# Performance work log

Hardware: AMD Instinct MI355X
Metric: run time of the kernel (lower is better)

## Reference

```python
import jax, jax.numpy as jnp
import numpy as np

B, T, U = 4, 512, 100
A_FEAT, TXT_FEAT, HID, NCLS = 512, 320, 640, 512


def setup_inputs() -> dict:
    key = jax.random.key(0)
    ks = jax.random.split(key, 8)
    s = lambda fan_in: 1.0 / np.sqrt(fan_in)
    return {
        "audio_frame": jax.random.normal(ks[0], (B, T, A_FEAT), jnp.float32),
        "text_frame": jax.random.normal(ks[1], (B, U, TXT_FEAT), jnp.float32),
        "W_a": jax.random.uniform(ks[2], (A_FEAT, HID), jnp.float32, -s(A_FEAT), s(A_FEAT)),
        "b_a": jax.random.uniform(ks[3], (HID,), jnp.float32, -s(A_FEAT), s(A_FEAT)),
        "W_t": jax.random.uniform(ks[4], (TXT_FEAT, HID), jnp.float32, -s(TXT_FEAT), s(TXT_FEAT)),
        "b_t": jax.random.uniform(ks[5], (HID,), jnp.float32, -s(TXT_FEAT), s(TXT_FEAT)),
        "W_j": jax.random.uniform(ks[6], (HID, NCLS), jnp.float32, -s(HID), s(HID)),
        "b_j": jax.random.uniform(ks[7], (NCLS,), jnp.float32, -s(HID), s(HID)),
    }


def reference(audio_frame, text_frame, W_a, b_a, W_t, b_t, W_j, b_j):
    # [B,T,H] and [B,U,H] projections
    a = jnp.einsum("bta,ah->bth", audio_frame, W_a) + b_a
    t = jnp.einsum("bux,xh->buh", text_frame, W_t) + b_t
    # broadcast add -> [B,T,U,H], tanh, final linear -> [B,T,U,V]
    joint = jnp.tanh(a[:, :, None, :] + t[:, None, :, :])
    return jnp.einsum("btuh,hv->btuv", joint, W_j) + b_j
```

## Files before the change

kernel.cpp:

```cpp
#include <hip/hip_runtime.h>
#include <hip/hip_bf16.h>
#include <stdint.h>

#define BB   4
#define TT   512
#define UU   100
#define AF   512
#define TXF  320
#define HID  640
#define NCLS 512
#define TU   (TT * UU)
#define M3   (BB * TU)

typedef unsigned short ushort_t;
typedef __attribute__((ext_vector_type(8))) short frag_ab;
typedef __attribute__((ext_vector_type(4))) float frag_cd;
typedef __attribute__((ext_vector_type(8))) unsigned short ushort8;

__device__ __forceinline__ float bf2f(unsigned short h) {
    return __uint_as_float(((unsigned)h) << 16);
}
__device__ __forceinline__ unsigned short f2bf(float f) {
    unsigned u = __float_as_uint(f);
    u += 0x7FFFu + ((u >> 16) & 1u);
    return (unsigned short)(u >> 16);
}
__device__ __forceinline__ float tanh_fast(float x) {
    float e = __expf(2.0f * x);
    return 1.0f - 2.0f * __builtin_amdgcn_rcpf(e + 1.0f);
}

__global__ void tcast_kernel(const float* __restrict__ src, ushort_t* __restrict__ dst,
                             int K, int N) {
    int i = blockIdx.x * 256 + threadIdx.x;
    if (i >= K * N) return;
    int k = i / N;
    int n = i - k * N;
    dst[n * K + k] = f2bf(src[i]);
}

__global__ __launch_bounds__(256) void proj_kernel(
    const float* __restrict__ X, const ushort_t* __restrict__ Wt,
    const float* __restrict__ bias, ushort_t* __restrict__ P,
    int M, int K)
{
    __shared__ ushort_t As[128][72];
    __shared__ ushort_t Bs[128][72];
    int tid = threadIdx.x;
    int m0 = blockIdx.x * 128, n0 = blockIdx.y * 128;
    int wave = tid >> 6, lane = tid & 63;
    int wr = (wave >> 1) * 64, wc = (wave & 1) * 64;
    int lm = lane & 15, lq = lane >> 4;
    frag_cd acc[4][4];
    #pragma unroll
    for (int i = 0; i < 4; ++i)
        #pragma unroll
        for (int j = 0; j < 4; ++j) { frag_cd z = {0.f, 0.f, 0.f, 0.f}; acc[i][j] = z; }
    int rs = tid >> 3, k8 = tid & 7;

    for (int k0 = 0; k0 < K; k0 += 64) {
        #pragma unroll
        for (int it = 0; it < 4; ++it) {
            int r = rs + it * 32;
            int m = m0 + r;
            float4 v0 = make_float4(0.f, 0.f, 0.f, 0.f), v1 = v0;
            if (m < M) {
                const float* xp = X + (size_t)m * K + (k0 + k8 * 8);
                v0 = *(const float4*)xp;
                v1 = *(const float4*)(xp + 4);
            }
            ushort8 o;
            o[0] = f2bf(v0.x); o[1] = f2bf(v0.y); o[2] = f2bf(v0.z); o[3] = f2bf(v0.w);
            o[4] = f2bf(v1.x); o[5] = f2bf(v1.y); o[6] = f2bf(v1.z); o[7] = f2bf(v1.w);
            *(ushort8*)&As[r][k8 * 8] = o;
            uint4 w = *(const uint4*)(Wt + (size_t)(n0 + r) * K + (k0 + k8 * 8));
            *(uint4*)&Bs[r][k8 * 8] = w;
        }
        __syncthreads();
        #pragma unroll
        for (int kk = 0; kk < 64; kk += 32) {
            frag_ab af[4], bfr[4];
            #pragma unroll
            for (int i = 0; i < 4; ++i) af[i]  = *(const frag_ab*)&As[wr + i * 16 + lm][kk + lq * 8];
            #pragma unroll
            for (int j = 0; j < 4; ++j) bfr[j] = *(const frag_ab*)&Bs[wc + j * 16 + lm][kk + lq * 8];
            #pragma unroll
            for (int i = 0; i < 4; ++i)
                #pragma unroll
                for (int j = 0; j < 4; ++j)
                    acc[i][j] = __builtin_amdgcn_mfma_f32_16x16x32_bf16(af[i], bfr[j], acc[i][j], 0, 0, 0);
        }
        __syncthreads();
    }
    #pragma unroll
    for (int j = 0; j < 4; ++j) {
        int n = n0 + wc + j * 16 + lm;
        float bv = bias[n];
        #pragma unroll
        for (int i = 0; i < 4; ++i) {
            int mb = m0 + wr + i * 16 + lq * 4;
            #pragma unroll
            for (int r = 0; r < 4; ++r) {
                int m = mb + r;
                if (m < M) P[(size_t)m * HID + n] = f2bf(acc[i][j][r] + bv);
            }
        }
    }
}

__global__ __launch_bounds__(256, 2) void joint_kernel(
    const ushort_t* __restrict__ Pa, const ushort_t* __restrict__ Pt,
    const ushort_t* __restrict__ Wtj, const float* __restrict__ bj,
    float* __restrict__ out)
{
    __shared__ ushort_t As[128][72];
    __shared__ ushort_t Bs[256][72];
    __shared__ int aOff[128];
    __shared__ int tOff[128];
    int tid = threadIdx.x;
    int m0 = blockIdx.x * 128;
    int n0 = blockIdx.y * 256;
    if (tid < 128) {
        int m  = m0 + tid;
        int b  = m / TU;
        int rb = m - b * TU;
        int ti = rb / UU;
        int ui = rb - ti * UU;
        aOff[tid] = (b * TT + ti) * HID;
        tOff[tid] = (b * UU + ui) * HID;
    }
    int wave = tid >> 6, lane = tid & 63;
    int wr = (wave >> 1) * 64;
    int wc = (wave & 1) * 128;
    int lm = lane & 15, lq = lane >> 4;
    frag_cd acc[4][8];
    #pragma unroll
    for (int i = 0; i < 4; ++i)
        #pragma unroll
        for (int j = 0; j < 8; ++j) { frag_cd z = {0.f, 0.f, 0.f, 0.f}; acc[i][j] = z; }
    int rs = tid >> 3, k8 = tid & 7;
    __syncthreads();

    for (int k0 = 0; k0 < HID; k0 += 64) {
        #pragma unroll
        for (int it = 0; it < 4; ++it) {
            int r = rs + it * 32;
            const ushort_t* ap = Pa + aOff[r] + k0 + k8 * 8;
            const ushort_t* tp = Pt + tOff[r] + k0 + k8 * 8;
            uint4 av = *(const uint4*)ap;
            uint4 tv = *(const uint4*)tp;
            const unsigned* au = (const unsigned*)&av;
            const unsigned* tu = (const unsigned*)&tv;
            ushort8 o;
            #pragma unroll
            for (int j = 0; j < 4; ++j) {
                unsigned ua = au[j], ut = tu[j];
                float s0 = __uint_as_float(ua << 16) + __uint_as_float(ut << 16);
                float s1 = __uint_as_float(ua & 0xFFFF0000u) + __uint_as_float(ut & 0xFFFF0000u);
                o[2 * j]     = f2bf(tanh_fast(s0));
                o[2 * j + 1] = f2bf(tanh_fast(s1));
            }
            *(ushort8*)&As[r][k8 * 8] = o;
        }
        #pragma unroll
        for (int it = 0; it < 8; ++it) {
            int r = rs + it * 32;
            *(uint4*)&Bs[r][k8 * 8] = *(const uint4*)(Wtj + (size_t)(n0 + r) * HID + k0 + k8 * 8);
        }
        __syncthreads();
        #pragma unroll
        for (int kk = 0; kk < 64; kk += 32) {
            frag_ab af[4], bfr[8];
            #pragma unroll
            for (int i = 0; i < 4; ++i) af[i]  = *(const frag_ab*)&As[wr + i * 16 + lm][kk + lq * 8];
            #pragma unroll
            for (int j = 0; j < 8; ++j) bfr[j] = *(const frag_ab*)&Bs[wc + j * 16 + lm][kk + lq * 8];
            #pragma unroll
            for (int i = 0; i < 4; ++i)
                #pragma unroll
                for (int j = 0; j < 8; ++j)
                    acc[i][j] = __builtin_amdgcn_mfma_f32_16x16x32_bf16(af[i], bfr[j], acc[i][j], 0, 0, 0);
        }
        __syncthreads();
    }
    #pragma unroll
    for (int j = 0; j < 8; ++j) {
        int n = n0 + wc + j * 16 + lm;
        float bv = bj[n];
        #pragma unroll
        for (int i = 0; i < 4; ++i) {
            size_t mb = (size_t)(m0 + wr + i * 16 + lq * 4);
            #pragma unroll
            for (int r = 0; r < 4; ++r) {
                out[(mb + r) * (size_t)NCLS + n] = acc[i][j][r] + bv;
            }
        }
    }
}

extern "C" void kernel_launch(void* const* d_in, const int* in_sizes, int n_in,
                              void* d_out, int out_size, void* d_ws, size_t ws_size,
                              hipStream_t stream)
{
    const float* audio = (const float*)d_in[0];
    const float* text  = (const float*)d_in[1];
    const float* Wa    = (const float*)d_in[2];
    const float* ba    = (const float*)d_in[3];
    const float* Wt    = (const float*)d_in[4];
    const float* bt    = (const float*)d_in[5];
    const float* Wj    = (const float*)d_in[6];
    const float* bjv   = (const float*)d_in[7];
    float* out = (float*)d_out;

    char* ws = (char*)d_ws;
    ushort_t* Pa  = (ushort_t*)(ws);
    ushort_t* Pt  = (ushort_t*)(ws + 2621440);
    ushort_t* Wta = (ushort_t*)(ws + 3133440);
    ushort_t* Wtt = (ushort_t*)(ws + 3788800);
    ushort_t* Wtj = (ushort_t*)(ws + 4198400);

    tcast_kernel<<<dim3((AF * HID + 255) / 256), 256, 0, stream>>>(Wa, Wta, AF, HID);
    tcast_kernel<<<dim3((TXF * HID + 255) / 256), 256, 0, stream>>>(Wt, Wtt, TXF, HID);
    tcast_kernel<<<dim3((HID * NCLS + 255) / 256), 256, 0, stream>>>(Wj, Wtj, HID, NCLS);

    proj_kernel<<<dim3(16, 5), 256, 0, stream>>>(audio, Wta, ba, Pa, BB * TT, AF);
    proj_kernel<<<dim3(4, 5), 256, 0, stream>>>(text, Wtt, bt, Pt, BB * UU, TXF);

    joint_kernel<<<dim3(M3 / 128, NCLS / 256), 256, 0, stream>>>(Pa, Pt, Wtj, bjv, out);
}
```

Measured before the change: 639.4 us.

## Cover all classes per joint block and prefetch next K tile into registers

The joint kernel now uses 512-thread blocks that cover all 512 output classes at once. The tanh(a+t) activation tile is computed once per row block instead of twice, which halves the transcendental work and the Pa/Pt gathers. Global loads for the next K slice are issued into registers before the MFMA loop runs, so load latency overlaps compute. The tanh now uses exp2 with a prescaled constant. In exchange the LDS footprint is larger and register pressure is higher under launch_bounds(512,2), so occupancy may drop.

After: 802.0 us. 25.4% more time.

```diff
diff --git a/kernel.cpp b/kernel.cpp
--- a/kernel.cpp
+++ b/kernel.cpp
@@ -26,7 +26,7 @@
     return (unsigned short)(u >> 16);
 }
 __device__ __forceinline__ float tanh_fast(float x) {
-    float e = __expf(2.0f * x);
+    float e = __builtin_amdgcn_exp2f(x * 2.8853900817779268f);
     return 1.0f - 2.0f * __builtin_amdgcn_rcpf(e + 1.0f);
 }
 
@@ -108,18 +108,17 @@
     }
 }
 
-__global__ __launch_bounds__(256, 2) void joint_kernel(
+__global__ __launch_bounds__(512, 2) void joint_kernel(
     const ushort_t* __restrict__ Pa, const ushort_t* __restrict__ Pt,
     const ushort_t* __restrict__ Wtj, const float* __restrict__ bj,
     float* __restrict__ out)
 {
     __shared__ ushort_t As[128][72];
-    __shared__ ushort_t Bs[256][72];
+    __shared__ ushort_t Bs[512][72];
     __shared__ int aOff[128];
     __shared__ int tOff[128];
     int tid = threadIdx.x;
     int m0 = blockIdx.x * 128;
-    int n0 = blockIdx.y * 256;
     if (tid < 128) {
         int m  = m0 + tid;
         int b  = m / TU;
@@ -130,8 +129,8 @@
         tOff[tid] = (b * UU + ui) * HID;
     }
     int wave = tid >> 6, lane = tid & 63;
-    int wr = (wave >> 1) * 64;
-    int wc = (wave & 1) * 128;
+    int wr = (wave >> 2) * 64;
+    int wc = (wave & 3) * 128;
     int lm = lane & 15, lq = lane >> 4;
     frag_cd acc[4][8];
     #pragma unroll
@@ -141,16 +140,26 @@
     int rs = tid >> 3, k8 = tid & 7;
     __syncthreads();
 
+    const int aO0 = aOff[rs], aO1 = aOff[rs + 64];
+    const int tO0 = tOff[rs], tO1 = tOff[rs + 64];
+    const int kcol = k8 * 8;
+
+    uint4 bv[8];
+    uint4 av[2], tv[2];
+
+    #pragma unroll
+    for (int it = 0; it < 8; ++it)
+        bv[it] = *(const uint4*)(Wtj + (size_t)(rs + it * 64) * HID + kcol);
+    av[0] = *(const uint4*)(Pa + aO0 + kcol);
+    av[1] = *(const uint4*)(Pa + aO1 + kcol);
+    tv[0] = *(const uint4*)(Pt + tO0 + kcol);
+    tv[1] = *(const uint4*)(Pt + tO1 + kcol);
+
     for (int k0 = 0; k0 < HID; k0 += 64) {
         #pragma unroll
-        for (int it = 0; it < 4; ++it) {
-            int r = rs + it * 32;
-            const ushort_t* ap = Pa + aOff[r] + k0 + k8 * 8;
-            const ushort_t* tp = Pt + tOff[r] + k0 + k8 * 8;
-            uint4 av = *(const uint4*)ap;
-            uint4 tv = *(const uint4*)tp;
-            const unsigned* au = (const unsigned*)&av;
-            const unsigned* tu = (const unsigned*)&tv;
+        for (int it = 0; it < 2; ++it) {
+            const unsigned* au = (const unsigned*)&av[it];
+            const unsigned* tu = (const unsigned*)&tv[it];
             ushort8 o;
             #pragma unroll
             for (int j = 0; j < 4; ++j) {
@@ -160,14 +169,24 @@
                 o[2 * j]     = f2bf(tanh_fast(s0));
                 o[2 * j + 1] = f2bf(tanh_fast(s1));
             }
-            *(ushort8*)&As[r][k8 * 8] = o;
-        }
-        #pragma unroll
-        for (int it = 0; it < 8; ++it) {
-            int r = rs + it * 32;
-            *(uint4*)&Bs[r][k8 * 8] = *(const uint4*)(Wtj + (size_t)(n0 + r) * HID + k0 + k8 * 8);
-        }
-        __syncthreads();
+            *(ushort8*)&As[rs + it * 64][kcol] = o;
+        }
+        #pragma unroll
+        for (int it = 0; it < 8; ++it)
+            *(uint4*)&Bs[rs + it * 64][kcol] = bv[it];
+
+        if (k0 + 64 < HID) {
+            int kn = k0 + 64 + kcol;
+            #pragma unroll
+            for (int it = 0; it < 8; ++it)
+                bv[it] = *(const uint4*)(Wtj + (size_t)(rs + it * 64) * HID + kn);
+            av[0] = *(const uint4*)(Pa + aO0 + kn);
+            av[1] = *(const uint4*)(Pa + aO1 + kn);
+            tv[0] = *(const uint4*)(Pt + tO0 + kn);
+            tv[1] = *(const uint4*)(Pt + tO1 + kn);
+        }
+        __syncthreads();
+
         #pragma unroll
         for (int kk = 0; kk < 64; kk += 32) {
             frag_ab af[4], bfr[8];
@@ -183,16 +202,17 @@
         }
         __syncthreads();
     }
+
     #pragma unroll
     for (int j = 0; j < 8; ++j) {
-        int n = n0 + wc + j * 16 + lm;
-        float bv = bj[n];
+        int n = wc + j * 16 + lm;
+        float bvv = bj[n];
         #pragma unroll
         for (int i = 0; i < 4; ++i) {
             size_t mb = (size_t)(m0 + wr + i * 16 + lq * 4);
             #pragma unroll
             for (int r = 0; r < 4; ++r) {
-                out[(mb + r) * (size_t)NCLS + n] = acc[i][j][r] + bv;
+                out[(mb + r) * (size_t)NCLS + n] = acc[i][j][r] + bvv;
             }
         }
     }
@@ -226,5 +246,5 @@
     proj_kernel<<<dim3(16, 5), 256, 0, stream>>>(audio, Wta, ba, Pa, BB * TT, AF);
     proj_kernel<<<dim3(4, 5), 256, 0, stream>>>(text, Wtt, bt, Pt, BB * UU, TXF);
 
-    joint_kernel<<<dim3(M3 / 128, NCLS / 256), 256, 0, stream>>>(Pa, Pt, Wtj, bjv, out);
-}
+    joint_kernel<<<dim3(M3 / 128), 512, 0, stream>>>(Pa, Pt, Wtj, bjv, out);
+}
```
